# Optimization experiments

Hardware: AMD Instinct MI355X
Metric: run time of the kernel (lower is better)

## Reference

```python
import jax, jax.numpy as jnp
import numpy as np

B, N, C, H = 16, 4096, 384, 8
NH = N // H  # per-head patch chunk = 512


def setup_inputs() -> dict:
    key = jax.random.key(0)
    ks = jax.random.split(key, 5)
    s = 1.0 / np.sqrt(N)
    return {
        "x": jax.random.normal(ks[0], (B, N, C), dtype=jnp.float32),
        "wq": jax.random.normal(ks[1], (N, N), dtype=jnp.float32) * s,
        "wkv": jax.random.normal(ks[2], (2 * N, N), dtype=jnp.float32) * s,
        "wproj": jax.random.normal(ks[3], (N, N), dtype=jnp.float32) * s,
        "bproj": jax.random.normal(ks[4], (N,), dtype=jnp.float32) * s,
        "scale": jnp.ones((H, 1, 1), dtype=jnp.float32),
    }


def reference(x, wq, wkv, wproj, bproj, scale):
    # x: [B, N, C] -> token-mixing over patch dim N
    xt = jnp.swapaxes(x, -2, -1)                      # [B, C, N]
    q = jnp.einsum('bcn,mn->bcm', xt, wq)             # [B, C, N]
    kv = jnp.einsum('bcn,mn->bcm', xt, wkv)           # [B, C, 2N]
    q = q.reshape(B, C, H, NH).transpose(0, 2, 1, 3)  # [B, H, C, NH]
    kv = kv.reshape(B, C, 2, H, NH).transpose(2, 0, 3, 1, 4)  # [2, B, H, C, NH]
    k, v = kv[0], kv[1]
    q = q / jnp.linalg.norm(q, axis=-1, keepdims=True)
    k = k / jnp.linalg.norm(k, axis=-1, keepdims=True)
    # channel-reduction kernel trick: [B, H, 1, NH], scaled per head
    kernel_trick = (k * v).sum(axis=-2, keepdims=True) * scale
    o = q * kernel_trick                               # [B, H, C, NH]
    o = o.transpose(0, 2, 1, 3).reshape(B, C, N)       # [B, C, N]
    o = jax.nn.gelu(o, approximate=False)              # torch nn.GELU = exact erf
    o = jnp.einsum('bcn,mn->bcm', o, wproj) + bproj    # proj over patch dim
    return jnp.swapaxes(o, -2, -1)                     # [B, N, C]
```

## Files before the change

### kernel.cpp

```cpp
#include <hip/hip_runtime.h>
#include <hip/hip_bf16.h>
#include <math.h>
#include <stdint.h>

#define B_ 16
#define N_ 4096
#define C_ 384
#define H_ 8
#define NH_ 512

typedef __attribute__((ext_vector_type(8))) short short8;
typedef __attribute__((ext_vector_type(4))) float f32x4;

__device__ __forceinline__ unsigned short f2bf(float x) {
  uint32_t u = __builtin_bit_cast(uint32_t, x);
  uint32_t r = (u + 0x7fffu + ((u >> 16) & 1u)) >> 16;
  return (unsigned short)r;
}
__device__ __forceinline__ float bf2f(unsigned short u) {
  uint32_t v = ((uint32_t)u) << 16;
  return __builtin_bit_cast(float, v);
}

__device__ __forceinline__ void gl2lds16(const void* g, void* l) {
  __builtin_amdgcn_global_load_lds((__attribute__((address_space(1))) void*)g,
                                   (__attribute__((address_space(3))) void*)l,
                                   16, 0, 0);
}

__global__ void cvt_f32_bf16(const float* __restrict__ src,
                             unsigned short* __restrict__ dst, size_t n) {
  size_t i = ((size_t)blockIdx.x * blockDim.x + threadIdx.x) * 8;
  if (i >= n) return;
  float4 a = *(const float4*)(src + i);
  float4 b = *(const float4*)(src + i + 4);
  typedef __attribute__((ext_vector_type(8))) unsigned short u16x8;
  u16x8 o;
  o[0] = f2bf(a.x); o[1] = f2bf(a.y); o[2] = f2bf(a.z); o[3] = f2bf(a.w);
  o[4] = f2bf(b.x); o[5] = f2bf(b.y); o[6] = f2bf(b.z); o[7] = f2bf(b.w);
  *(u16x8*)(dst + i) = o;
}

__global__ __launch_bounds__(256)
void transpose_x(const float* __restrict__ x, unsigned short* __restrict__ xT) {
  __shared__ float tile[64 * 65];
  int b = blockIdx.z;
  int n0 = blockIdx.x * 64;
  int c0 = blockIdx.y * 64;
  int t = threadIdx.x;
  const float* xb = x + (size_t)b * N_ * C_;
  #pragma unroll
  for (int i = 0; i < 16; i++) {
    int r = i * 4 + (t >> 6);
    int cc = t & 63;
    tile[r * 65 + cc] = xb[(size_t)(n0 + r) * C_ + c0 + cc];
  }
  __syncthreads();
  unsigned short* xTb = xT + (size_t)b * C_ * N_;
  #pragma unroll
  for (int i = 0; i < 16; i++) {
    int r = i * 4 + (t >> 6);
    int nn = t & 63;
    xTb[(size_t)(c0 + r) * N_ + n0 + nn] = f2bf(tile[nn * 65 + r]);
  }
}

template <bool BIAS>
__global__ __launch_bounds__(256, 2)
void gemm_bt(const unsigned short* __restrict__ A,
             const unsigned short* __restrict__ Bt,
             void* __restrict__ OutV,
             const float* __restrict__ bias,
             size_t bStride, size_t outStride) {
  __shared__ unsigned short As[128 * 64];
  __shared__ unsigned short Bs[128 * 64];
  const int b  = blockIdx.x;
  const int m0 = blockIdx.y * 128;
  const int c0 = blockIdx.z * 128;
  const int t = threadIdx.x;
  const int lane = t & 63;
  const int w = t >> 6;
  const int wm = (w & 1) * 64;
  const int wn = (w >> 1) * 64;
  const int quad = lane >> 4;
  const int r16  = lane & 15;

  const unsigned short* Bb = Bt + (size_t)b * bStride;

  f32x4 acc[4][4];
  #pragma unroll
  for (int i = 0; i < 4; i++)
    #pragma unroll
    for (int j = 0; j < 4; j++)
      acc[i][j] = (f32x4){0.f, 0.f, 0.f, 0.f};

  const int rs = t >> 3;
  const int q8 = (t & 7) ^ (rs & 7);
  const unsigned short* aSrc = A  + (size_t)(m0 + rs) * 4096 + q8 * 8;
  const unsigned short* bSrc = Bb + (size_t)(c0 + rs) * 4096 + q8 * 8;
  unsigned short* aDst = As + t * 8;
  unsigned short* bDst = Bs + t * 8;

  for (int k0 = 0; k0 < 4096; k0 += 64) {
    #pragma unroll
    for (int p = 0; p < 4; p++) {
      gl2lds16(aSrc + (size_t)p * 32 * 4096 + k0, aDst + p * 2048);
      gl2lds16(bSrc + (size_t)p * 32 * 4096 + k0, bDst + p * 2048);
    }
    __syncthreads();
    #pragma unroll
    for (int kk = 0; kk < 2; kk++) {
      short8 af[4], bfv[4];
      const int cb = kk * 4 + quad;
      #pragma unroll
      for (int i = 0; i < 4; i++) {
        int ra = wm + i * 16 + r16;
        af[i]  = *(const short8*)(As + ra * 64 + ((cb ^ (ra & 7)) * 8));
        int rb = wn + i * 16 + r16;
        bfv[i] = *(const short8*)(Bs + rb * 64 + ((cb ^ (rb & 7)) * 8));
      }
      #pragma unroll
      for (int i = 0; i < 4; i++)
        #pragma unroll
        for (int j = 0; j < 4; j++)
          acc[i][j] = __builtin_amdgcn_mfma_f32_16x16x32_bf16(
              af[i], bfv[j], acc[i][j], 0, 0, 0);
    }
    __syncthreads();
  }

  if (BIAS) {
    float* Out = (float*)OutV + (size_t)b * outStride;
    #pragma unroll
    for (int i = 0; i < 4; i++) {
      #pragma unroll
      for (int v = 0; v < 4; v++) {
        int m = m0 + wm + i * 16 + quad * 4 + v;
        float bi = bias[m];
        #pragma unroll
        for (int j = 0; j < 4; j++) {
          int c = c0 + wn + j * 16 + r16;
          Out[(size_t)m * C_ + c] = acc[i][j][v] + bi;
        }
      }
    }
  } else {
    unsigned short* Out = (unsigned short*)OutV + (size_t)b * outStride;
    #pragma unroll
    for (int i = 0; i < 4; i++) {
      #pragma unroll
      for (int v = 0; v < 4; v++) {
        int m = m0 + wm + i * 16 + quad * 4 + v;
        #pragma unroll
        for (int j = 0; j < 4; j++) {
          int c = c0 + wn + j * 16 + r16;
          Out[(size_t)m * C_ + c] = f2bf(acc[i][j][v]);
        }
      }
    }
  }
}

__global__ __launch_bounds__(512)
void middle(const unsigned short* __restrict__ Y,
            unsigned short* __restrict__ GT,
            const float* __restrict__ scale) {
  const int h = blockIdx.x;
  const int b = blockIdx.y;
  const unsigned short* Yb = Y + (size_t)b * 12288 * C_;
  const unsigned short* Q = Yb + (size_t)(h * NH_) * C_;
  const unsigned short* K = Yb + (size_t)(N_ + h * NH_) * C_;
  const unsigned short* V = Yb + (size_t)(2 * N_ + h * NH_) * C_;
  unsigned short* GTb = GT + (size_t)b * C_ * N_ + h * NH_;

  __shared__ float invq[C_], invk[C_], kt[NH_];
  const int t = threadIdx.x;
  const float sc = scale[h];

  if (t < C_) {
    float sq = 0.f, sk = 0.f;
    for (int n = 0; n < NH_; n++) {
      float qv = bf2f(Q[(size_t)n * C_ + t]);
      float kv = bf2f(K[(size_t)n * C_ + t]);
      sq += qv * qv;
      sk += kv * kv;
    }
    invq[t] = rsqrtf(sq);
    invk[t] = rsqrtf(sk);
  }
  __syncthreads();

  {
    int w = t >> 6, l = t & 63;
    for (int n = w; n < NH_; n += 8) {
      float s = 0.f;
      for (int c = l; c < C_; c += 64)
        s += bf2f(K[(size_t)n * C_ + c]) * invk[c] * bf2f(V[(size_t)n * C_ + c]);
      #pragma unroll
      for (int o = 32; o > 0; o >>= 1) s += __shfl_xor(s, o);
      if (l == 0) kt[n] = s * sc;
    }
  }
  __syncthreads();

  {
    int n = t;
    float ktv = kt[n];
    for (int c = 0; c < C_; c++) {
      float xv = bf2f(Q[(size_t)n * C_ + c]) * invq[c] * ktv;
      float g = 0.5f * xv * (1.0f + erff(xv * 0.70710678118654752f));
      GTb[(size_t)c * N_ + n] = f2bf(g);
    }
  }
}

extern "C" void kernel_launch(void* const* d_in, const int* in_sizes, int n_in,
                              void* d_out, int out_size, void* d_ws, size_t ws_size,
                              hipStream_t stream) {
  const float* x     = (const float*)d_in[0];
  const float* wq    = (const float*)d_in[1];
  const float* wkv   = (const float*)d_in[2];
  const float* wproj = (const float*)d_in[3];
  const float* bproj = (const float*)d_in[4];
  const float* scale = (const float*)d_in[5];

  unsigned short* Wqkv = (unsigned short*)d_ws;
  unsigned short* Wp   = Wqkv + (size_t)12288 * 4096;
  unsigned short* xT   = Wp   + (size_t)4096 * 4096;
  unsigned short* Y    = xT   + (size_t)B_ * C_ * N_;
  unsigned short* GT   = Y    + (size_t)B_ * 12288 * C_;

  const size_t nq  = (size_t)4096 * 4096;
  const size_t nkv = (size_t)8192 * 4096;

  cvt_f32_bf16<<<(int)(nq  / 8 / 256), 256, 0, stream>>>(wq,    Wqkv,      nq);
  cvt_f32_bf16<<<(int)(nkv / 8 / 256), 256, 0, stream>>>(wkv,   Wqkv + nq, nkv);
  cvt_f32_bf16<<<(int)(nq  / 8 / 256), 256, 0, stream>>>(wproj, Wp,        nq);

  transpose_x<<<dim3(64, 6, 16), 256, 0, stream>>>(x, xT);

  gemm_bt<false><<<dim3(16, 96, 3), 256, 0, stream>>>(
      Wqkv, xT, Y, nullptr, (size_t)C_ * N_, (size_t)12288 * C_);

  middle<<<dim3(8, 16), 512, 0, stream>>>(Y, GT, scale);

  gemm_bt<true><<<dim3(16, 32, 3), 256, 0, stream>>>(
      Wp, GT, d_out, bproj, (size_t)C_ * N_, (size_t)N_ * C_);
}
```

Measured before the change: 1.386 ms.

## Enlarge GEMM tile to 256x128 with 512 threads and flatten batch into N

The GEMM kernel moves from a 128x128 tile with 4 waves to a 256x128 tile with 8 waves, so each B tile is reused across twice as many weight rows. The batch dimension is folded into the column index, and the grid becomes a flat 2D launch whose x index covers batch and channel tiles. Because consecutive blocks now share the same weight rows, this is meant to cut global and L2 traffic per FLOP and improve weight reuse in L2. In exchange, LDS use per block grows to 48KB and the launch bound of 4 blocks per CU caps registers per thread.

```diff
diff --git a/kernel.cpp b/kernel.cpp
--- a/kernel.cpp
+++ b/kernel.cpp
@@ -66,26 +66,24 @@
 }
 
 template <bool BIAS>
-__global__ __launch_bounds__(256, 2)
+__global__ __launch_bounds__(512, 4)
 void gemm_bt(const unsigned short* __restrict__ A,
              const unsigned short* __restrict__ Bt,
              void* __restrict__ OutV,
              const float* __restrict__ bias,
-             size_t bStride, size_t outStride) {
-  __shared__ unsigned short As[128 * 64];
+             size_t outBatchStride) {
+  __shared__ unsigned short As[256 * 64];
   __shared__ unsigned short Bs[128 * 64];
-  const int b  = blockIdx.x;
-  const int m0 = blockIdx.y * 128;
-  const int c0 = blockIdx.z * 128;
+  const int ct = blockIdx.x;
+  const int m0 = blockIdx.y * 256;
+  const int cg0 = ct * 128;
   const int t = threadIdx.x;
   const int lane = t & 63;
   const int w = t >> 6;
-  const int wm = (w & 1) * 64;
-  const int wn = (w >> 1) * 64;
+  const int wm = (w & 3) * 64;
+  const int wn = (w >> 2) * 64;
   const int quad = lane >> 4;
   const int r16  = lane & 15;
-
-  const unsigned short* Bb = Bt + (size_t)b * bStride;
 
   f32x4 acc[4][4];
   #pragma unroll
@@ -97,16 +95,17 @@
   const int rs = t >> 3;
   const int q8 = (t & 7) ^ (rs & 7);
   const unsigned short* aSrc = A  + (size_t)(m0 + rs) * 4096 + q8 * 8;
-  const unsigned short* bSrc = Bb + (size_t)(c0 + rs) * 4096 + q8 * 8;
+  const unsigned short* bSrc = Bt + (size_t)(cg0 + rs) * 4096 + q8 * 8;
   unsigned short* aDst = As + t * 8;
   unsigned short* bDst = Bs + t * 8;
 
   for (int k0 = 0; k0 < 4096; k0 += 64) {
     #pragma unroll
-    for (int p = 0; p < 4; p++) {
-      gl2lds16(aSrc + (size_t)p * 32 * 4096 + k0, aDst + p * 2048);
-      gl2lds16(bSrc + (size_t)p * 32 * 4096 + k0, bDst + p * 2048);
-    }
+    for (int p = 0; p < 4; p++)
+      gl2lds16(aSrc + (size_t)p * 64 * 4096 + k0, aDst + p * 4096);
+    #pragma unroll
+    for (int p = 0; p < 2; p++)
+      gl2lds16(bSrc + (size_t)p * 64 * 4096 + k0, bDst + p * 4096);
     __syncthreads();
     #pragma unroll
     for (int kk = 0; kk < 2; kk++) {
@@ -129,8 +128,11 @@
     __syncthreads();
   }
 
+  const int bb = ct / 3;
+  const int cbase = (ct - bb * 3) * 128;
+
   if (BIAS) {
-    float* Out = (float*)OutV + (size_t)b * outStride;
+    float* Out = (float*)OutV + (size_t)bb * outBatchStride;
     #pragma unroll
     for (int i = 0; i < 4; i++) {
       #pragma unroll
@@ -139,13 +141,13 @@
         float bi = bias[m];
         #pragma unroll
         for (int j = 0; j < 4; j++) {
-          int c = c0 + wn + j * 16 + r16;
+          int c = cbase + wn + j * 16 + r16;
           Out[(size_t)m * C_ + c] = acc[i][j][v] + bi;
         }
       }
     }
   } else {
-    unsigned short* Out = (unsigned short*)OutV + (size_t)b * outStride;
+    unsigned short* Out = (unsigned short*)OutV + (size_t)bb * outBatchStride;
     #pragma unroll
     for (int i = 0; i < 4; i++) {
       #pragma unroll
@@ -153,7 +155,7 @@
         int m = m0 + wm + i * 16 + quad * 4 + v;
         #pragma unroll
         for (int j = 0; j < 4; j++) {
-          int c = c0 + wn + j * 16 + r16;
+          int c = cbase + wn + j * 16 + r16;
           Out[(size_t)m * C_ + c] = f2bf(acc[i][j][v]);
         }
       }
@@ -239,11 +241,11 @@
 
   transpose_x<<<dim3(64, 6, 16), 256, 0, stream>>>(x, xT);
 
-  gemm_bt<false><<<dim3(16, 96, 3), 256, 0, stream>>>(
-      Wqkv, xT, Y, nullptr, (size_t)C_ * N_, (size_t)12288 * C_);
+  gemm_bt<false><<<dim3(48, 48), 512, 0, stream>>>(
+      Wqkv, xT, Y, nullptr, (size_t)12288 * C_);
 
   middle<<<dim3(8, 16), 512, 0, stream>>>(Y, GT, scale);
 
-  gemm_bt<true><<<dim3(16, 32, 3), 256, 0, stream>>>(
-      Wp, GT, d_out, bproj, (size_t)C_ * N_, (size_t)N_ * C_);
-}
+  gemm_bt<true><<<dim3(48, 16), 512, 0, stream>>>(
+      Wp, GT, d_out, bproj, (size_t)N_ * C_);
+}
```

New measurement: 1.442 ms. 1.04x slower.
